# Kernel optimization log

Measured on AMD Instinct MI355X. Metric: run time of the kernel, lower is better.

## Reference

```python
import jax, jax.numpy as jnp
import numpy as np

N_NODES = 50000
N_EDGES = 800000
HIDDEN = 128
EDGE_DIM = 4
N_LAYERS = 4
MLP_HID = 64


def setup_inputs() -> dict:
    key = jax.random.key(0)
    ks = jax.random.split(key, 12)
    inp = {
        "x": jax.random.normal(ks[0], (N_NODES, 1), dtype=jnp.float32),
        "edge_index": jax.random.randint(ks[1], (2, N_EDGES), 0, N_NODES, dtype=jnp.int64),
        "edge_attr": jax.random.normal(ks[2], (N_EDGES, EDGE_DIM), dtype=jnp.float32),
        # embed: Linear(1, HIDDEN)
        "embed_w": jax.random.normal(ks[3], (1, HIDDEN), dtype=jnp.float32) * 0.5,
        "embed_b": jnp.zeros((HIDDEN,), dtype=jnp.float32),
        # per-layer edge MLP: Linear(EDGE_DIM,64) -> ReLU -> Linear(64,1) -> Softplus
        "ew1": jax.random.normal(ks[4], (N_LAYERS, EDGE_DIM, MLP_HID), dtype=jnp.float32) * (1.0 / np.sqrt(EDGE_DIM)),
        "eb1": jnp.zeros((N_LAYERS, MLP_HID), dtype=jnp.float32),
        "ew2": jax.random.normal(ks[5], (N_LAYERS, MLP_HID, 1), dtype=jnp.float32) * (1.0 / np.sqrt(MLP_HID)),
        "eb2": jnp.zeros((N_LAYERS, 1), dtype=jnp.float32),
        # out head: Linear(H,H) -> ReLU -> Linear(H,1)
        "out_w1": jax.random.normal(ks[6], (HIDDEN, HIDDEN), dtype=jnp.float32) * (1.0 / np.sqrt(HIDDEN)),
        "out_b1": jnp.zeros((HIDDEN,), dtype=jnp.float32),
        "out_w2": jax.random.normal(ks[7], (HIDDEN, 1), dtype=jnp.float32) * (1.0 / np.sqrt(HIDDEN)),
        "out_b2": jnp.zeros((1,), dtype=jnp.float32),
    }
    return inp


def reference(x, edge_index, edge_attr, embed_w, embed_b, ew1, eb1, ew2, eb2,
              out_w1, out_b1, out_w2, out_b2):
    n_nodes = x.shape[0]
    src = edge_index[0]  # x_j (source, PyG flow source_to_target)
    dst = edge_index[1]  # x_i (target, aggregation index)

    h = x @ embed_w + embed_b  # [N, H]
    n_layers = ew1.shape[0]
    for l in range(n_layers):
        # edge MLP -> scalar conductivity k_ij per edge, softplus-positive
        hmid = jax.nn.relu(edge_attr @ ew1[l] + eb1[l])       # [E, 64]
        k = jax.nn.softplus(hmid @ ew2[l] + eb2[l])           # [E, 1]
        msg = k * (h[src] - h[dst])                            # [E, H]
        h = jax.ops.segment_sum(msg, dst, num_segments=n_nodes)  # [N, H]

    out = jax.nn.relu(h @ out_w1 + out_b1) @ out_w2 + out_b2  # [N, 1]
    return out
```

## Files before the change

### kernel.cpp

```cpp
#include <hip/hip_runtime.h>
#include <math.h>

#define NN 50000
#define NE 800000
#define HD 128
#define ED 4
#define NL 4
#define MH 64
#define NE2 (NE / 2)
#define NBIN 196
#define BINCAP 8192
#define CURSTRIDE 16
#define NBF 782
#define NMLPB 1563

__device__ __forceinline__ float softplus_f(float a) {
    return fmaxf(a, 0.0f) + __logf(1.0f + __expf(-fabsf(a)));
}

__device__ __forceinline__ void mlp_layer(
    int l, int t,
    const float* __restrict__ edge_attr,
    const float* __restrict__ ew1, const float* __restrict__ eb1,
    const float* __restrict__ ew2, const float* __restrict__ eb2,
    float* __restrict__ k_all)
{
    if (t >= NE2) return;
    const int e0 = t, e1 = t + NE2;
    const float4 a0 = *reinterpret_cast<const float4*>(edge_attr + (size_t)e0 * 4);
    const float4 a1 = *reinterpret_cast<const float4*>(edge_attr + (size_t)e1 * 4);

    const float* __restrict__ W0 = ew1 + (size_t)(l * ED + 0) * MH;
    const float* __restrict__ W1 = ew1 + (size_t)(l * ED + 1) * MH;
    const float* __restrict__ W2 = ew1 + (size_t)(l * ED + 2) * MH;
    const float* __restrict__ W3 = ew1 + (size_t)(l * ED + 3) * MH;
    const float* __restrict__ B1 = eb1 + (size_t)l * MH;
    const float* __restrict__ V2 = ew2 + (size_t)l * MH;

    float p0 = 0.0f, q0 = 0.0f, p1 = 0.0f, q1 = 0.0f;
    #pragma unroll 4
    for (int j = 0; j < MH; j += 2) {
        {
            const float w0 = W0[j], w1 = W1[j], w2 = W2[j], w3 = W3[j];
            const float b1 = B1[j], v2 = V2[j];
            float m0 = fmaf(a0.x, w0, fmaf(a0.y, w1, fmaf(a0.z, w2, fmaf(a0.w, w3, b1))));
            float m1 = fmaf(a1.x, w0, fmaf(a1.y, w1, fmaf(a1.z, w2, fmaf(a1.w, w3, b1))));
            p0 = fmaf(fmaxf(m0, 0.0f), v2, p0);
            p1 = fmaf(fmaxf(m1, 0.0f), v2, p1);
        }
        {
            const float w0 = W0[j+1], w1 = W1[j+1], w2 = W2[j+1], w3 = W3[j+1];
            const float b1 = B1[j+1], v2 = V2[j+1];
            float m0 = fmaf(a0.x, w0, fmaf(a0.y, w1, fmaf(a0.z, w2, fmaf(a0.w, w3, b1))));
            float m1 = fmaf(a1.x, w0, fmaf(a1.y, w1, fmaf(a1.z, w2, fmaf(a1.w, w3, b1))));
            q0 = fmaf(fmaxf(m0, 0.0f), v2, q0);
            q1 = fmaf(fmaxf(m1, 0.0f), v2, q1);
        }
    }
    const float bb = eb2[l];
    k_all[(size_t)l * NE + e0] = softplus_f(bb + (p0 + q0));
    k_all[(size_t)l * NE + e1] = softplus_f(bb + (p1 + q1));
}

__global__ __launch_bounds__(256) void fill_mlp0_kernel(
    const int* __restrict__ eidx,
    int* __restrict__ gcur,
    int2* __restrict__ gbin,
    const float* __restrict__ edge_attr,
    const float* __restrict__ ew1, const float* __restrict__ eb1,
    const float* __restrict__ ew2, const float* __restrict__ eb2,
    float* __restrict__ k_all)
{
    __shared__ int hist[NBIN];
    __shared__ int base[NBIN];

    if (blockIdx.x < NBF) {
        int tid = threadIdx.x;
        if (tid < NBIN) hist[tid] = 0;
        __syncthreads();

        int e0 = (blockIdx.x * 256 + tid) * 4;
        int bin[4], dloc[4], rank[4];
        int4 srcs, dsts;
        bool act = e0 < NE;
        if (act) {
            srcs = *reinterpret_cast<const int4*>(eidx + e0);
            dsts = *reinterpret_cast<const int4*>(eidx + NE + e0);
            int dd[4] = {dsts.x, dsts.y, dsts.z, dsts.w};
            #pragma unroll
            for (int i = 0; i < 4; ++i) {
                bin[i]  = dd[i] >> 8;
                dloc[i] = dd[i] & 255;
                rank[i] = atomicAdd(&hist[bin[i]], 1);
            }
        }
        __syncthreads();
        if (tid < NBIN && hist[tid]) base[tid] = atomicAdd(&gcur[tid * CURSTRIDE], hist[tid]);
        __syncthreads();
        if (act) {
            int ss[4] = {srcs.x, srcs.y, srcs.z, srcs.w};
            #pragma unroll
            for (int i = 0; i < 4; ++i) {
                int pos = bin[i] * BINCAP + base[bin[i]] + rank[i];
                gbin[pos] = make_int2(ss[i], (dloc[i] << 20) | (e0 + i));
            }
        }
        return;
    }

    int t = (blockIdx.x - NBF) * 256 + threadIdx.x;
    mlp_layer(0, t, edge_attr, ew1, eb1, ew2, eb2, k_all);
}

__global__ __launch_bounds__(256) void csr_mlp123_kernel(
    const int* __restrict__ gcur,
    const int2* __restrict__ gbin,
    int2* __restrict__ gsorted,
    int2* __restrict__ nodeSD,
    const float* __restrict__ edge_attr,
    const float* __restrict__ ew1, const float* __restrict__ eb1,
    const float* __restrict__ ew2, const float* __restrict__ eb2,
    float* __restrict__ k_all)
{
    __shared__ int cnt[256];
    __shared__ int cur[256];
    __shared__ int wsum[4];
    __shared__ int woff[4];

    if (blockIdx.x < NBIN) {
        int b = blockIdx.x;
        int tid = threadIdx.x;
        int lane = tid & 63;
        int wid = tid >> 6;
        int m = gcur[b * CURSTRIDE];
        const int2* src = gbin + (size_t)b * BINCAP;

        cnt[tid] = 0;
        __syncthreads();
        for (int p = tid; p < m; p += 256) {
            int dloc = src[p].y >> 20;
            atomicAdd(&cnt[dloc], 1);
        }
        __syncthreads();
        int v = cnt[tid];
        int x = v;
        #pragma unroll
        for (int o = 1; o < 64; o <<= 1) {
            int t = __shfl_up(x, o);
            if (lane >= o) x += t;
        }
        if (lane == 63) wsum[wid] = x;
        __syncthreads();
        if (tid == 0) {
            int a = 0;
            #pragma unroll
            for (int w = 0; w < 4; ++w) { woff[w] = a; a += wsum[w]; }
        }
        __syncthreads();
        int excl = x + woff[wid] - v;
        cur[tid] = excl;
        int n = (b << 8) + tid;
        if (n < NN) nodeSD[n] = make_int2(b * BINCAP + excl, v);
        __syncthreads();
        for (int p = tid; p < m; p += 256) {
            int2 r = src[p];
            int dloc = r.y >> 20;
            int q = atomicAdd(&cur[dloc], 1);
            gsorted[(size_t)b * BINCAP + q] = make_int2(r.x, r.y & 0xFFFFF);
        }
        return;
    }

    int lb = blockIdx.x - NBIN;
    int l  = 1 + lb / NMLPB;
    int t  = (lb - (l - 1) * NMLPB) * 256 + threadIdx.x;
    mlp_layer(l, t, edge_attr, ew1, eb1, ew2, eb2, k_all);
}

__global__ void sgather_kernel(const int2* __restrict__ nodeSD,
                               const int2* __restrict__ gsorted,
                               const float* __restrict__ k_all,
                               int l,
                               const float* __restrict__ s_in,
                               float* __restrict__ s_out) {
    int t = blockIdx.x * 256 + threadIdx.x;
    int n = t >> 4;
    int gl = threadIdx.x & 15;
    if (n >= NN) return;
    int2 sd = nodeSD[n];
    float sk = 0.0f, sks = 0.0f;
    for (int p = gl; p < sd.y; p += 16) {
        int2 r = gsorted[sd.x + p];
        float kk = k_all[(size_t)l * NE + r.y];
        sk += kk;
        sks = fmaf(kk, s_in[r.x], sks);
    }
    #pragma unroll
    for (int m = 1; m < 16; m <<= 1) {
        sk  += __shfl_xor(sk, m);
        sks += __shfl_xor(sks, m);
    }
    if (gl == 0) s_out[n] = fmaf(-sk, s_in[n], sks);
}

__global__ void sgather_head_kernel(const int2* __restrict__ nodeSD,
                                    const int2* __restrict__ gsorted,
                                    const float* __restrict__ k_all,
                                    const float* __restrict__ s_in,
                                    const float* __restrict__ ew,
                                    const float* __restrict__ ow1,
                                    const float* __restrict__ b1,
                                    const float* __restrict__ w2,
                                    const float* __restrict__ b2,
                                    float* __restrict__ out) {
    __shared__ float su[HD], sb1[HD], sw2[HD];
    if (threadIdx.x < HD) {
        int j = threadIdx.x;
        float a = 0.0f;
        #pragma unroll 8
        for (int c = 0; c < HD; ++c) a = fmaf(ew[c], ow1[c * HD + j], a);
        su[j]  = a;
        sb1[j] = b1[j];
        sw2[j] = w2[j];
    }
    __syncthreads();

    int t = blockIdx.x * 256 + threadIdx.x;
    int n = t >> 4;
    int gl = threadIdx.x & 15;
    if (n >= NN) return;
    int2 sd = nodeSD[n];
    float sk = 0.0f, sks = 0.0f;
    for (int p = gl; p < sd.y; p += 16) {
        int2 r = gsorted[sd.x + p];
        float kk = k_all[3 * (size_t)NE + r.y];
        sk += kk;
        sks = fmaf(kk, s_in[r.x], sks);
    }
    #pragma unroll
    for (int m = 1; m < 16; m <<= 1) {
        sk  += __shfl_xor(sk, m);
        sks += __shfl_xor(sks, m);
    }
    float sv = fmaf(-sk, s_in[n], sks);

    float acc = 0.0f;
    #pragma unroll
    for (int jj = 0; jj < 8; ++jj) {
        int j = gl + jj * 16;
        acc = fmaf(fmaxf(fmaf(sv, su[j], sb1[j]), 0.0f), sw2[j], acc);
    }
    #pragma unroll
    for (int m = 1; m < 16; m <<= 1) acc += __shfl_xor(acc, m);
    if (gl == 0) out[n] = acc + b2[0];
}


extern "C" void kernel_launch(void* const* d_in, const int* in_sizes, int n_in,
                              void* d_out, int out_size, void* d_ws, size_t ws_size,
                              hipStream_t stream) {
    const float* x        = (const float*)d_in[0];
    const int*   eidx     = (const int*)d_in[1];
    const float* edge_attr= (const float*)d_in[2];
    const float* embed_w  = (const float*)d_in[3];
    const float* ew1      = (const float*)d_in[5];
    const float* eb1      = (const float*)d_in[6];
    const float* ew2      = (const float*)d_in[7];
    const float* eb2      = (const float*)d_in[8];
    const float* ow1      = (const float*)d_in[9];
    const float* ob1      = (const float*)d_in[10];
    const float* ow2      = (const float*)d_in[11];
    const float* ob2      = (const float*)d_in[12];
    float* out = (float*)d_out;

    char* ws = (char*)d_ws;
    const size_t kbytes  = (size_t)NL * NE * sizeof(float);
    const size_t gbbytes = (size_t)NBIN * BINCAP * sizeof(int2);
    const size_t curbyte = (size_t)NBIN * CURSTRIDE * sizeof(int);
    const size_t sdbytes = (size_t)NN * sizeof(int2);
    const size_t sbytes  = (size_t)NN * sizeof(float);

    size_t off = 0;
    float* k_all   = (float*)(ws + off); off += kbytes;
    int2*  gbin    = (int2*) (ws + off); off += gbbytes;
    int2*  gsorted = (int2*) (ws + off); off += gbbytes;
    int*   gcur    = (int*)  (ws + off); off += curbyte;
    int2*  nodeSD  = (int2*) (ws + off); off += sdbytes;
    float* sA      = (float*)(ws + off); off += sbytes;
    float* sB      = (float*)(ws + off); off += sbytes;

    hipMemsetAsync(gcur, 0, curbyte, stream);

    fill_mlp0_kernel<<<NBF + NMLPB, 256, 0, stream>>>(
        eidx, gcur, gbin, edge_attr, ew1, eb1, ew2, eb2, k_all);

    csr_mlp123_kernel<<<NBIN + 3 * NMLPB, 256, 0, stream>>>(
        gcur, gbin, gsorted, nodeSD, edge_attr, ew1, eb1, ew2, eb2, k_all);

    const int ggrid = (NN * 16 + 255) / 256;
    sgather_kernel<<<ggrid, 256, 0, stream>>>(nodeSD, gsorted, k_all, 0, x,  sA);
    sgather_kernel<<<ggrid, 256, 0, stream>>>(nodeSD, gsorted, k_all, 1, sA, sB);
    sgather_kernel<<<ggrid, 256, 0, stream>>>(nodeSD, gsorted, k_all, 2, sB, sA);
    sgather_head_kernel<<<ggrid, 256, 0, stream>>>(nodeSD, gsorted, k_all, sA,
                                                   embed_w, ow1, ob1, ow2, ob2, out);
}
```

Before: 121.8 us.

## Fuse layer-0 gather into CSR build blocks and process four edges per MLP thread

```diff
diff --git a/kernel.cpp b/kernel.cpp
--- a/kernel.cpp
+++ b/kernel.cpp
@@ -7,12 +7,12 @@
 #define ED 4
 #define NL 4
 #define MH 64
-#define NE2 (NE / 2)
+#define NE4 (NE / 4)
 #define NBIN 196
 #define BINCAP 8192
 #define CURSTRIDE 16
 #define NBF 782
-#define NMLPB 1563
+#define NMLPB 782
 
 __device__ __forceinline__ float softplus_f(float a) {
     return fmaxf(a, 0.0f) + __logf(1.0f + __expf(-fabsf(a)));
@@ -25,10 +25,12 @@
     const float* __restrict__ ew2, const float* __restrict__ eb2,
     float* __restrict__ k_all)
 {
-    if (t >= NE2) return;
-    const int e0 = t, e1 = t + NE2;
+    if (t >= NE4) return;
+    const int e0 = t, e1 = t + NE4, e2 = t + 2 * NE4, e3 = t + 3 * NE4;
     const float4 a0 = *reinterpret_cast<const float4*>(edge_attr + (size_t)e0 * 4);
     const float4 a1 = *reinterpret_cast<const float4*>(edge_attr + (size_t)e1 * 4);
+    const float4 a2 = *reinterpret_cast<const float4*>(edge_attr + (size_t)e2 * 4);
+    const float4 a3 = *reinterpret_cast<const float4*>(edge_attr + (size_t)e3 * 4);
 
     const float* __restrict__ W0 = ew1 + (size_t)(l * ED + 0) * MH;
     const float* __restrict__ W1 = ew1 + (size_t)(l * ED + 1) * MH;
@@ -37,29 +39,25 @@
     const float* __restrict__ B1 = eb1 + (size_t)l * MH;
     const float* __restrict__ V2 = ew2 + (size_t)l * MH;
 
-    float p0 = 0.0f, q0 = 0.0f, p1 = 0.0f, q1 = 0.0f;
-    #pragma unroll 4
-    for (int j = 0; j < MH; j += 2) {
-        {
-            const float w0 = W0[j], w1 = W1[j], w2 = W2[j], w3 = W3[j];
-            const float b1 = B1[j], v2 = V2[j];
-            float m0 = fmaf(a0.x, w0, fmaf(a0.y, w1, fmaf(a0.z, w2, fmaf(a0.w, w3, b1))));
-            float m1 = fmaf(a1.x, w0, fmaf(a1.y, w1, fmaf(a1.z, w2, fmaf(a1.w, w3, b1))));
-            p0 = fmaf(fmaxf(m0, 0.0f), v2, p0);
-            p1 = fmaf(fmaxf(m1, 0.0f), v2, p1);
-        }
-        {
-            const float w0 = W0[j+1], w1 = W1[j+1], w2 = W2[j+1], w3 = W3[j+1];
-            const float b1 = B1[j+1], v2 = V2[j+1];
-            float m0 = fmaf(a0.x, w0, fmaf(a0.y, w1, fmaf(a0.z, w2, fmaf(a0.w, w3, b1))));
-            float m1 = fmaf(a1.x, w0, fmaf(a1.y, w1, fmaf(a1.z, w2, fmaf(a1.w, w3, b1))));
-            q0 = fmaf(fmaxf(m0, 0.0f), v2, q0);
-            q1 = fmaf(fmaxf(m1, 0.0f), v2, q1);
-        }
+    float acc0 = 0.0f, acc1 = 0.0f, acc2 = 0.0f, acc3 = 0.0f;
+    #pragma unroll 8
+    for (int j = 0; j < MH; ++j) {
+        const float w0 = W0[j], w1 = W1[j], w2 = W2[j], w3 = W3[j];
+        const float b1 = B1[j], v2 = V2[j];
+        float m0 = fmaf(a0.x, w0, fmaf(a0.y, w1, fmaf(a0.z, w2, fmaf(a0.w, w3, b1))));
+        float m1 = fmaf(a1.x, w0, fmaf(a1.y, w1, fmaf(a1.z, w2, fmaf(a1.w, w3, b1))));
+        float m2 = fmaf(a2.x, w0, fmaf(a2.y, w1, fmaf(a2.z, w2, fmaf(a2.w, w3, b1))));
+        float m3 = fmaf(a3.x, w0, fmaf(a3.y, w1, fmaf(a3.z, w2, fmaf(a3.w, w3, b1))));
+        acc0 = fmaf(fmaxf(m0, 0.0f), v2, acc0);
+        acc1 = fmaf(fmaxf(m1, 0.0f), v2, acc1);
+        acc2 = fmaf(fmaxf(m2, 0.0f), v2, acc2);
+        acc3 = fmaf(fmaxf(m3, 0.0f), v2, acc3);
     }
     const float bb = eb2[l];
-    k_all[(size_t)l * NE + e0] = softplus_f(bb + (p0 + q0));
-    k_all[(size_t)l * NE + e1] = softplus_f(bb + (p1 + q1));
+    k_all[(size_t)l * NE + e0] = softplus_f(bb + acc0);
+    k_all[(size_t)l * NE + e1] = softplus_f(bb + acc1);
+    k_all[(size_t)l * NE + e2] = softplus_f(bb + acc2);
+    k_all[(size_t)l * NE + e3] = softplus_f(bb + acc3);
 }
 
 __global__ __launch_bounds__(256) void fill_mlp0_kernel(
@@ -112,15 +110,17 @@
     mlp_layer(0, t, edge_attr, ew1, eb1, ew2, eb2, k_all);
 }
 
-__global__ __launch_bounds__(256) void csr_mlp123_kernel(
+__global__ __launch_bounds__(256) void csr_g0_mlp123_kernel(
     const int* __restrict__ gcur,
     const int2* __restrict__ gbin,
     int2* __restrict__ gsorted,
     int2* __restrict__ nodeSD,
+    float* __restrict__ k_all,
+    const float* __restrict__ x,
+    float* __restrict__ sA,
     const float* __restrict__ edge_attr,
     const float* __restrict__ ew1, const float* __restrict__ eb1,
-    const float* __restrict__ ew2, const float* __restrict__ eb2,
-    float* __restrict__ k_all)
+    const float* __restrict__ ew2, const float* __restrict__ eb2)
 {
     __shared__ int cnt[256];
     __shared__ int cur[256];
@@ -143,13 +143,13 @@
         }
         __syncthreads();
         int v = cnt[tid];
-        int x = v;
+        int xx = v;
         #pragma unroll
         for (int o = 1; o < 64; o <<= 1) {
-            int t = __shfl_up(x, o);
-            if (lane >= o) x += t;
-        }
-        if (lane == 63) wsum[wid] = x;
+            int t = __shfl_up(xx, o);
+            if (lane >= o) xx += t;
+        }
+        if (lane == 63) wsum[wid] = xx;
         __syncthreads();
         if (tid == 0) {
             int a = 0;
@@ -157,7 +157,7 @@
             for (int w = 0; w < 4; ++w) { woff[w] = a; a += wsum[w]; }
         }
         __syncthreads();
-        int excl = x + woff[wid] - v;
+        int excl = xx + woff[wid] - v;
         cur[tid] = excl;
         int n = (b << 8) + tid;
         if (n < NN) nodeSD[n] = make_int2(b * BINCAP + excl, v);
@@ -167,6 +167,30 @@
             int dloc = r.y >> 20;
             int q = atomicAdd(&cur[dloc], 1);
             gsorted[(size_t)b * BINCAP + q] = make_int2(r.x, r.y & 0xFFFFF);
+        }
+
+        __threadfence();
+        __syncthreads();
+        int g  = tid >> 4;
+        int gl = tid & 15;
+        for (int i = 0; i < 16; ++i) {
+            int nl  = i * 16 + g;
+            int n2  = (b << 8) + nl;
+            int deg = cnt[nl];
+            int st  = cur[nl] - deg;
+            float sk = 0.0f, sks = 0.0f;
+            for (int p = gl; p < deg; p += 16) {
+                int2 r = gsorted[(size_t)b * BINCAP + st + p];
+                float kk = k_all[r.y];
+                sk += kk;
+                sks = fmaf(kk, x[r.x], sks);
+            }
+            #pragma unroll
+            for (int mm = 1; mm < 16; mm <<= 1) {
+                sk  += __shfl_xor(sk, mm);
+                sks += __shfl_xor(sks, mm);
+            }
+            if (gl == 0 && n2 < NN) sA[n2] = fmaf(-sk, x[n2], sks);
         }
         return;
     }
@@ -294,11 +318,11 @@
     fill_mlp0_kernel<<<NBF + NMLPB, 256, 0, stream>>>(
         eidx, gcur, gbin, edge_attr, ew1, eb1, ew2, eb2, k_all);
 
-    csr_mlp123_kernel<<<NBIN + 3 * NMLPB, 256, 0, stream>>>(
-        gcur, gbin, gsorted, nodeSD, edge_attr, ew1, eb1, ew2, eb2, k_all);
+    csr_g0_mlp123_kernel<<<NBIN + 3 * NMLPB, 256, 0, stream>>>(
+        gcur, gbin, gsorted, nodeSD, k_all, x, sA,
+        edge_attr, ew1, eb1, ew2, eb2);
 
     const int ggrid = (NN * 16 + 255) / 256;
-    sgather_kernel<<<ggrid, 256, 0, stream>>>(nodeSD, gsorted, k_all, 0, x,  sA);
     sgather_kernel<<<ggrid, 256, 0, stream>>>(nodeSD, gsorted, k_all, 1, sA, sB);
     sgather_kernel<<<ggrid, 256, 0, stream>>>(nodeSD, gsorted, k_all, 2, sB, sA);
     sgather_head_kernel<<<ggrid, 256, 0, stream>>>(nodeSD, gsorted, k_all, sA,
```

New measurement: 154.3 us. 26.7% more time.

## Interleave later-layer edge MLP work into gather kernels

Applied to the files above, without the earlier changes.

```diff
diff --git a/kernel.cpp b/kernel.cpp
--- a/kernel.cpp
+++ b/kernel.cpp
@@ -13,6 +13,10 @@
 #define CURSTRIDE 16
 #define NBF 782
 #define NMLPB 1563
+#define SGBLK 3125
+#define L3A 782
+#define L3B 781
+#define L3OFF 200192
 
 __device__ __forceinline__ float softplus_f(float a) {
     return fmaxf(a, 0.0f) + __logf(1.0f + __expf(-fabsf(a)));
@@ -112,7 +116,7 @@
     mlp_layer(0, t, edge_attr, ew1, eb1, ew2, eb2, k_all);
 }
 
-__global__ __launch_bounds__(256) void csr_mlp123_kernel(
+__global__ __launch_bounds__(256) void csr_mlp1_kernel(
     const int* __restrict__ gcur,
     const int2* __restrict__ gbin,
     int2* __restrict__ gsorted,
@@ -143,13 +147,13 @@
         }
         __syncthreads();
         int v = cnt[tid];
-        int x = v;
+        int xx = v;
         #pragma unroll
         for (int o = 1; o < 64; o <<= 1) {
-            int t = __shfl_up(x, o);
-            if (lane >= o) x += t;
-        }
-        if (lane == 63) wsum[wid] = x;
+            int t = __shfl_up(xx, o);
+            if (lane >= o) xx += t;
+        }
+        if (lane == 63) wsum[wid] = xx;
         __syncthreads();
         if (tid == 0) {
             int a = 0;
@@ -157,7 +161,7 @@
             for (int w = 0; w < 4; ++w) { woff[w] = a; a += wsum[w]; }
         }
         __syncthreads();
-        int excl = x + woff[wid] - v;
+        int excl = xx + woff[wid] - v;
         cur[tid] = excl;
         int n = (b << 8) + tid;
         if (n < NN) nodeSD[n] = make_int2(b * BINCAP + excl, v);
@@ -171,36 +175,47 @@
         return;
     }
 
-    int lb = blockIdx.x - NBIN;
-    int l  = 1 + lb / NMLPB;
-    int t  = (lb - (l - 1) * NMLPB) * 256 + threadIdx.x;
-    mlp_layer(l, t, edge_attr, ew1, eb1, ew2, eb2, k_all);
-}
-
-__global__ void sgather_kernel(const int2* __restrict__ nodeSD,
-                               const int2* __restrict__ gsorted,
-                               const float* __restrict__ k_all,
-                               int l,
-                               const float* __restrict__ s_in,
-                               float* __restrict__ s_out) {
-    int t = blockIdx.x * 256 + threadIdx.x;
-    int n = t >> 4;
-    int gl = threadIdx.x & 15;
-    if (n >= NN) return;
-    int2 sd = nodeSD[n];
-    float sk = 0.0f, sks = 0.0f;
-    for (int p = gl; p < sd.y; p += 16) {
-        int2 r = gsorted[sd.x + p];
-        float kk = k_all[(size_t)l * NE + r.y];
-        sk += kk;
-        sks = fmaf(kk, s_in[r.x], sks);
-    }
-    #pragma unroll
-    for (int m = 1; m < 16; m <<= 1) {
-        sk  += __shfl_xor(sk, m);
-        sks += __shfl_xor(sks, m);
-    }
-    if (gl == 0) s_out[n] = fmaf(-sk, s_in[n], sks);
+    int t = (blockIdx.x - NBIN) * 256 + threadIdx.x;
+    mlp_layer(1, t, edge_attr, ew1, eb1, ew2, eb2, k_all);
+}
+
+__global__ __launch_bounds__(256) void sg_mlp_kernel(
+    const int2* __restrict__ nodeSD,
+    const int2* __restrict__ gsorted,
+    float* k_all,
+    int lg,
+    const float* __restrict__ s_in,
+    float* __restrict__ s_out,
+    int lp, int tpad0,
+    const float* __restrict__ edge_attr,
+    const float* __restrict__ ew1, const float* __restrict__ eb1,
+    const float* __restrict__ ew2, const float* __restrict__ eb2)
+{
+    if (blockIdx.x < SGBLK) {
+        int t = blockIdx.x * 256 + threadIdx.x;
+        int n = t >> 4;
+        int gl = threadIdx.x & 15;
+        if (n >= NN) return;
+        int2 sd = nodeSD[n];
+        float sk = 0.0f, sks = 0.0f;
+        const float* kl = k_all + (size_t)lg * NE;
+        for (int p = gl; p < sd.y; p += 16) {
+            int2 r = gsorted[sd.x + p];
+            float kk = kl[r.y];
+            sk += kk;
+            sks = fmaf(kk, s_in[r.x], sks);
+        }
+        #pragma unroll
+        for (int m = 1; m < 16; m <<= 1) {
+            sk  += __shfl_xor(sk, m);
+            sks += __shfl_xor(sks, m);
+        }
+        if (gl == 0) s_out[n] = fmaf(-sk, s_in[n], sks);
+        return;
+    }
+
+    int t = tpad0 + (blockIdx.x - SGBLK) * 256 + threadIdx.x;
+    mlp_layer(lp, t, edge_attr, ew1, eb1, ew2, eb2, k_all);
 }
 
 __global__ void sgather_head_kernel(const int2* __restrict__ nodeSD,
@@ -294,13 +309,21 @@
     fill_mlp0_kernel<<<NBF + NMLPB, 256, 0, stream>>>(
         eidx, gcur, gbin, edge_attr, ew1, eb1, ew2, eb2, k_all);
 
-    csr_mlp123_kernel<<<NBIN + 3 * NMLPB, 256, 0, stream>>>(
+    csr_mlp1_kernel<<<NBIN + NMLPB, 256, 0, stream>>>(
         gcur, gbin, gsorted, nodeSD, edge_attr, ew1, eb1, ew2, eb2, k_all);
 
-    const int ggrid = (NN * 16 + 255) / 256;
-    sgather_kernel<<<ggrid, 256, 0, stream>>>(nodeSD, gsorted, k_all, 0, x,  sA);
-    sgather_kernel<<<ggrid, 256, 0, stream>>>(nodeSD, gsorted, k_all, 1, sA, sB);
-    sgather_kernel<<<ggrid, 256, 0, stream>>>(nodeSD, gsorted, k_all, 2, sB, sA);
-    sgather_head_kernel<<<ggrid, 256, 0, stream>>>(nodeSD, gsorted, k_all, sA,
+    sg_mlp_kernel<<<SGBLK + NMLPB, 256, 0, stream>>>(
+        nodeSD, gsorted, k_all, 0, x, sA, 2, 0,
+        edge_attr, ew1, eb1, ew2, eb2);
+
+    sg_mlp_kernel<<<SGBLK + L3A, 256, 0, stream>>>(
+        nodeSD, gsorted, k_all, 1, sA, sB, 3, 0,
+        edge_attr, ew1, eb1, ew2, eb2);
+
+    sg_mlp_kernel<<<SGBLK + L3B, 256, 0, stream>>>(
+        nodeSD, gsorted, k_all, 2, sB, sA, 3, L3OFF,
+        edge_attr, ew1, eb1, ew2, eb2);
+
+    sgather_head_kernel<<<SGBLK, 256, 0, stream>>>(nodeSD, gsorted, k_all, sA,
                                                    embed_w, ow1, ob1, ow2, ob2, out);
 }
```

Result: slower. 129.6 us (+6.4%).
